# Performance work log

Hardware: AMD Instinct MI355X
Metric: run time of the kernel (lower is better)

## Reference

```python
import jax, jax.numpy as jnp
import numpy as np

NU, NM, FEAT, E, EL, H, ED, C = 50000, 20000, 32, 262144, 100000, 512, 7, 7


def _seg_mean(msg, dst, n):
    # scatter-mean aggregation (PyG SAGEConv default aggr='mean'; empty segments -> 0)
    s = jax.ops.segment_sum(msg, dst, num_segments=n)
    cnt = jax.ops.segment_sum(jnp.ones(dst.shape, msg.dtype), dst, num_segments=n)
    return s / jnp.maximum(cnt, 1.0)[:, None]


def _conv(x_src, x_dst, ei, ea, lw, lb, rw, ew, eb):
    # EdgeSAGEConv: message = x_j + edge_lin(edge_attr); out = lin_l(mean-aggr) + lin_r(x_dst)
    msg = x_src[ei[0]] + ea @ ew + eb            # [E, H]
    agg = _seg_mean(msg, ei[1], x_dst.shape[0])  # [N_dst, H]
    return agg @ lw + lb + x_dst @ rw


def setup_inputs() -> dict:
    key = jax.random.key(0)
    ks = iter(jax.random.split(key, 40))

    def rn(shape, scale=1.0):
        return jax.random.normal(next(ks), shape, jnp.float32) * scale

    inp = {}
    inp["movie_x"] = rn((NM, FEAT))
    inp["user_emb_w"] = rn((NU, H))
    inp["movie_emb_w"] = rn((NM, H))
    inp["movie_lin_w"] = rn((FEAT, H), FEAT ** -0.5)
    inp["movie_lin_b"] = jnp.zeros((H,), jnp.float32)
    inp["edge_attr_um"] = rn((E, ED))
    inp["edge_attr_mu"] = rn((E, ED))
    for p in ("mu1", "um1", "mu2", "um2"):
        inp[p + "_lin_l_w"] = rn((H, H), H ** -0.5)
        inp[p + "_lin_l_b"] = jnp.zeros((H,), jnp.float32)
        inp[p + "_lin_r_w"] = rn((H, H), H ** -0.5)
        inp[p + "_edge_w"] = rn((ED, H), ED ** -0.5)
        inp[p + "_edge_b"] = jnp.zeros((H,), jnp.float32)
    inp["cls_w"] = rn((2 * H, C), (2 * H) ** -0.5)
    inp["cls_b"] = jnp.zeros((C,), jnp.float32)
    inp["edge_index_um"] = jnp.stack([
        jax.random.randint(next(ks), (E,), 0, NU),
        jax.random.randint(next(ks), (E,), 0, NM)])
    inp["edge_index_mu"] = jnp.stack([
        jax.random.randint(next(ks), (E,), 0, NM),
        jax.random.randint(next(ks), (E,), 0, NU)])
    inp["edge_label_index"] = jnp.stack([
        jax.random.randint(next(ks), (EL,), 0, NU),
        jax.random.randint(next(ks), (EL,), 0, NM)])
    return inp


def reference(movie_x, user_emb_w, movie_emb_w, movie_lin_w, movie_lin_b,
              edge_attr_um, edge_attr_mu,
              mu1_lin_l_w, mu1_lin_l_b, mu1_lin_r_w, mu1_edge_w, mu1_edge_b,
              um1_lin_l_w, um1_lin_l_b, um1_lin_r_w, um1_edge_w, um1_edge_b,
              mu2_lin_l_w, mu2_lin_l_b, mu2_lin_r_w, mu2_edge_w, mu2_edge_b,
              um2_lin_l_w, um2_lin_l_b, um2_lin_r_w, um2_edge_w, um2_edge_b,
              cls_w, cls_b,
              edge_index_um, edge_index_mu, edge_label_index):
    # node encoders (node_id == arange -> embedding table used directly)
    x_u = user_emb_w                                             # [NU, H]
    x_m = movie_x @ movie_lin_w + movie_lin_b + movie_emb_w      # [NM, H]
    # hetero layer 1 (one edge type per destination node type)
    u1 = jax.nn.relu(_conv(x_m, x_u, edge_index_mu, edge_attr_mu,
                           mu1_lin_l_w, mu1_lin_l_b, mu1_lin_r_w, mu1_edge_w, mu1_edge_b))
    m1 = jax.nn.relu(_conv(x_u, x_m, edge_index_um, edge_attr_um,
                           um1_lin_l_w, um1_lin_l_b, um1_lin_r_w, um1_edge_w, um1_edge_b))
    # hetero layer 2
    u2 = _conv(m1, u1, edge_index_mu, edge_attr_mu,
               mu2_lin_l_w, mu2_lin_l_b, mu2_lin_r_w, mu2_edge_w, mu2_edge_b)
    m2 = _conv(u1, m1, edge_index_um, edge_attr_um,
               um2_lin_l_w, um2_lin_l_b, um2_lin_r_w, um2_edge_w, um2_edge_b)
    # edge classifier
    feat = jnp.concatenate([u2[edge_label_index[0]], m2[edge_label_index[1]]], axis=-1)
    return feat @ cls_w + cls_b
```

## Files before the change

kernel.cpp:

```cpp
#include <hip/hip_runtime.h>
#include <hip/hip_bf16.h>

#define NUU 50000
#define NMM 20000
#define NT (NUU + NMM)
#define FEAT 32
#define NE 262144
#define NEL 100000
#define HD 512
#define EDIM 7
#define NC 7

typedef __hip_bfloat16 bf16;
typedef __attribute__((ext_vector_type(8))) short short8;
typedef __attribute__((ext_vector_type(4))) float f32x4;

__device__ __forceinline__ float b2f(unsigned short u)
{
  return __uint_as_float((unsigned)u << 16);
}
__device__ __forceinline__ unsigned short f2bbits(float x)
{
  __hip_bfloat16 h = __float2bfloat16(x);
  return *reinterpret_cast<unsigned short*>(&h);
}
__device__ __forceinline__ float2 ld2(const float* p) { return *(const float2*)p; }
__device__ __forceinline__ void st2b(bf16* p, float x, float y)
{
  ushort2 u = make_ushort2(f2bbits(x), f2bbits(y));
  *(ushort2*)p = u;
}
__device__ __forceinline__ void gload16(const void* g, void* l)
{
  __builtin_amdgcn_global_load_lds(
      (const __attribute__((address_space(1))) void*)g,
      (__attribute__((address_space(3))) void*)l, 16, 0, 0);
}

__global__ __launch_bounds__(256) void prep_k(
    const float* __restrict__ mx, const float* __restrict__ W,
    const float* __restrict__ b, const float* __restrict__ emb,
    bf16* __restrict__ xm, const float* __restrict__ uin, bf16* __restrict__ ubf)
{
  const int tid = threadIdx.x;
  if (blockIdx.x < 1024) {
    const int c0 = 2 * tid;
    float2 wreg[FEAT];
#pragma unroll
    for (int k = 0; k < FEAT; ++k) wreg[k] = ld2(&W[(size_t)k * HD + c0]);
    const float2 bv = ld2(&b[c0]);
    __shared__ float xr[FEAT];
    for (int m = blockIdx.x; m < NMM; m += 1024) {
      if (tid < FEAT) xr[tid] = mx[(size_t)m * FEAT + tid];
      __syncthreads();
      float2 e2 = ld2(&emb[(size_t)m * HD + c0]);
      float s0 = bv.x + e2.x, s1 = bv.y + e2.y;
#pragma unroll
      for (int k = 0; k < FEAT; ++k) {
        s0 += xr[k] * wreg[k].x;
        s1 += xr[k] * wreg[k].y;
      }
      st2b(&xm[(size_t)m * HD + c0], s0, s1);
      __syncthreads();
    }
  } else {
    const int n4 = NUU * HD / 4;
    for (int i = (blockIdx.x - 1024) * 256 + tid; i < n4; i += 1024 * 256) {
      float4 v = *(const float4*)&uin[4 * (size_t)i];
      ushort4 u = make_ushort4(f2bbits(v.x), f2bbits(v.y), f2bbits(v.z), f2bbits(v.w));
      *(ushort4*)&ubf[4 * (size_t)i] = u;
    }
  }
}

__global__ __launch_bounds__(256) void wtrans_k(
    const float* __restrict__ lwA, const float* __restrict__ rwA, bf16* __restrict__ WcA,
    const float* __restrict__ lwB, const float* __restrict__ rwB, bf16* __restrict__ WcB)
{
  const float* lw = blockIdx.z ? lwB : lwA;
  const float* rw = blockIdx.z ? rwB : rwA;
  bf16* Wcat = blockIdx.z ? WcB : WcA;
  __shared__ float s[32][33];
  const int tx = threadIdx.x & 31;
  const int ty = threadIdx.x >> 5;
  const int nt = blockIdx.x * 32;
  const int kt = blockIdx.y * 32;
#pragma unroll
  for (int q = 0; q < 4; ++q) {
    int k = kt + q * 8 + ty;
    int n = nt + tx;
    float v = (k < HD) ? lw[(size_t)k * HD + n] : rw[(size_t)(k - HD) * HD + n];
    s[q * 8 + ty][tx] = v;
  }
  __syncthreads();
#pragma unroll
  for (int q = 0; q < 4; ++q) {
    int n = nt + q * 8 + ty;
    int k = kt + tx;
    Wcat[(size_t)n * (2 * HD) + k] = __float2bfloat16(s[tx][q * 8 + ty]);
  }
}

__global__ void count2_k(const int* __restrict__ dmu, const int* __restrict__ dum,
                         int* __restrict__ cnt)
{
  for (int i = blockIdx.x * blockDim.x + threadIdx.x; i < NE; i += gridDim.x * blockDim.x) {
    atomicAdd(&cnt[dmu[i]], 1);
    atomicAdd(&cnt[NUU + dum[i]], 1);
  }
}

__global__ __launch_bounds__(512) void scan_a512(const int* __restrict__ in,
                                                 int* __restrict__ out,
                                                 int* __restrict__ bsum, int n)
{
  __shared__ int s[512];
  const int tid = threadIdx.x;
  const int i = blockIdx.x * 512 + tid;
  int v = (i < n) ? in[i] : 0;
  s[tid] = v;
  __syncthreads();
  for (int d = 1; d < 512; d <<= 1) {
    int t = (tid >= d) ? s[tid - d] : 0;
    __syncthreads();
    s[tid] += t;
    __syncthreads();
  }
  if (i < n) out[i] = s[tid] - v;
  if (tid == 511) bsum[blockIdx.x] = s[511];
}

__global__ void scan_b256(int* __restrict__ bsum, int nb)
{
  __shared__ int s[256];
  const int tid = threadIdx.x;
  int v = (tid < nb) ? bsum[tid] : 0;
  s[tid] = v;
  __syncthreads();
  for (int d = 1; d < 256; d <<= 1) {
    int t = (tid >= d) ? s[tid - d] : 0;
    __syncthreads();
    s[tid] += t;
    __syncthreads();
  }
  if (tid < nb) bsum[tid] = s[tid] - v;
}

__global__ __launch_bounds__(512) void scan_c512(int* __restrict__ out,
                                                 const int* __restrict__ bsum, int n)
{
  const int i = blockIdx.x * 512 + threadIdx.x;
  if (i < n) out[i] += bsum[blockIdx.x];
}

__global__ void fill2_k(const int* __restrict__ smu, const int* __restrict__ dmu,
                        const int* __restrict__ sum_, const int* __restrict__ dum,
                        const int* __restrict__ off, int* __restrict__ fill,
                        int* __restrict__ csrE, int* __restrict__ csrS)
{
  for (int i = blockIdx.x * blockDim.x + threadIdx.x; i < NE; i += gridDim.x * blockDim.x) {
    int d0 = dmu[i];
    int p0 = off[d0] + atomicAdd(&fill[d0], 1);
    csrE[p0] = i;
    csrS[p0] = smu[i];
    int d1 = NUU + dum[i];
    int p1 = off[d1] + atomicAdd(&fill[d1], 1);
    csrE[p1] = i;
    csrS[p1] = sum_[i];
  }
}

__global__ __launch_bounds__(256) void easum2_k(
    const float* __restrict__ eaMU, const float* __restrict__ eaUM,
    const int* __restrict__ csrE, const int* __restrict__ off,
    const int* __restrict__ cnt, float* __restrict__ eaSum)
{
  const int g = threadIdx.x >> 3;
  const int cl = threadIdx.x & 7;
  const int d = blockIdx.x * 32 + g;
  if (d >= NT) return;
  const float* __restrict__ ea = (d < NUU) ? eaMU : eaUM;
  const int deg = cnt[d];
  const int start = off[d];
  float a = 0.f;
  for (int i = 0; i < deg; ++i) {
    int e = csrE[start + i];
    if (cl < 7) a += ea[(size_t)e * EDIM + cl];
  }
  eaSum[(size_t)d * 8 + cl] = (cl < 7) ? a : 0.f;
}

__global__ __launch_bounds__(64) void projw_k(
    const float* __restrict__ lwA, const float* __restrict__ rwA,
    const float* __restrict__ lbA, const float* __restrict__ clsW,
    float* __restrict__ WlA, float* __restrict__ WrA, float* __restrict__ ccA,
    const float* __restrict__ lwB, const float* __restrict__ rwB,
    const float* __restrict__ lbB,
    float* __restrict__ WlB, float* __restrict__ WrB, float* __restrict__ ccB)
{
  const int side = blockIdx.y;
  const float* lw = side ? lwB : lwA;
  const float* rw = side ? rwB : rwA;
  const float* lb = side ? lbB : lbA;
  const float* cw = clsW + (side ? (size_t)HD * NC : 0);
  float* Wl = side ? WlB : WlA;
  float* Wr = side ? WrB : WrA;
  float* cc = side ? ccB : ccA;
  const int k = blockIdx.x;
  const int l = threadIdx.x;
  if (k < HD) {
    float aL[NC] = {0, 0, 0, 0, 0, 0, 0};
    float aR[NC] = {0, 0, 0, 0, 0, 0, 0};
    for (int j = l; j < HD; j += 64) {
      float a = lw[(size_t)k * HD + j];
      float b = rw[(size_t)k * HD + j];
#pragma unroll
      for (int c = 0; c < NC; ++c) {
        float w = cw[(size_t)j * NC + c];
        aL[c] += a * w;
        aR[c] += b * w;
      }
    }
#pragma unroll
    for (int c = 0; c < NC; ++c)
      for (int s = 32; s; s >>= 1) {
        aL[c] += __shfl_xor(aL[c], s);
        aR[c] += __shfl_xor(aR[c], s);
      }
    if (l == 0) {
#pragma unroll
      for (int c = 0; c < NC; ++c) {
        Wl[k * NC + c] = aL[c];
        Wr[k * NC + c] = aR[c];
      }
    }
  } else {
    float a0[NC] = {0, 0, 0, 0, 0, 0, 0};
    for (int j = l; j < HD; j += 64) {
      float a = lb[j];
#pragma unroll
      for (int c = 0; c < NC; ++c) a0[c] += a * cw[(size_t)j * NC + c];
    }
#pragma unroll
    for (int c = 0; c < NC; ++c)
      for (int s = 32; s; s >>= 1) a0[c] += __shfl_xor(a0[c], s);
    if (l == 0) {
#pragma unroll
      for (int c = 0; c < NC; ++c) cc[c] = a0[c];
    }
  }
}

__global__ __launch_bounds__(512) void proj2_k(
    const float* __restrict__ ewA, const float* __restrict__ ebA,
    const float* __restrict__ WlA, float* __restrict__ ewPA, float* __restrict__ ebPA,
    const float* __restrict__ ewB, const float* __restrict__ ebB,
    const float* __restrict__ WlB, float* __restrict__ ewPB, float* __restrict__ ebPB)
{
  const int side = blockIdx.x;
  const float* ew = side ? ewB : ewA;
  const float* ebv = side ? ebB : ebA;
  const float* Wl = side ? WlB : WlA;
  float* ewP = side ? ewPB : ewPA;
  float* ebP = side ? ebPB : ebPA;
  const int j = threadIdx.x >> 6;
  const int l = threadIdx.x & 63;
  const float* __restrict__ src = (j < 7) ? &ew[(size_t)j * HD] : ebv;
  float acc[NC] = {0, 0, 0, 0, 0, 0, 0};
  for (int k = l; k < HD; k += 64) {
    float v = src[k];
#pragma unroll
    for (int c = 0; c < NC; ++c) acc[c] += v * Wl[(size_t)k * NC + c];
  }
#pragma unroll
  for (int c = 0; c < NC; ++c)
    for (int s = 32; s; s >>= 1) acc[c] += __shfl_xor(acc[c], s);
  if (l == 0) {
    if (j < 7) {
#pragma unroll
      for (int c = 0; c < NC; ++c) ewP[j * 8 + c] = acc[c];
      ewP[j * 8 + 7] = 0.f;
    } else {
#pragma unroll
      for (int c = 0; c < NC; ++c) ebP[c] = acc[c];
      ebP[7] = 0.f;
    }
  }
}

__global__ __launch_bounds__(256) void w2t_k(
    const float* __restrict__ WAu, const float* __restrict__ WBu, bf16* __restrict__ W2u,
    const float* __restrict__ WAm, const float* __restrict__ WBm, bf16* __restrict__ W2m)
{
  int idx = blockIdx.x * 256 + threadIdx.x;
  if (idx >= 2 * 16 * HD) return;
  const int side = idx >= 16 * HD;
  if (side) idx -= 16 * HD;
  const float* WA = side ? WAm : WAu;
  const float* WB = side ? WBm : WBu;
  bf16* W2t = side ? W2m : W2u;
  int n = idx >> 9;
  int k = idx & (HD - 1);
  float v = 0.f;
  if (n < 7) v = WA[k * NC + n];
  else if (n >= 8 && n < 15) v = WB[k * NC + (n - 8)];
  W2t[(size_t)n * HD + k] = __float2bfloat16(v);
}

__global__ __launch_bounds__(256) void agg_all_k(
    const float* __restrict__ mPa, const float* __restrict__ uPb,
    const float* __restrict__ uPa, const float* __restrict__ mPb,
    const int* __restrict__ csrS, const int* __restrict__ off,
    const int* __restrict__ cnt, const float* __restrict__ eaSum,
    const float* __restrict__ ewP_u, const float* __restrict__ ebP_u,
    const float* __restrict__ cc_u, const float* __restrict__ ewP_m,
    const float* __restrict__ ebP_m, const float* __restrict__ cc_m,
    float* __restrict__ Pu, float* __restrict__ Pm)
{
  const int g = threadIdx.x >> 3;
  const int cl = threadIdx.x & 7;
  const int d = blockIdx.x * 32 + g;
  if (d >= NT) return;
  const int user = (d < NUU);
  const float* srcP = user ? mPa : uPa;
  const float* ownP = user ? uPb : mPb;
  const float* ewP = user ? ewP_u : ewP_m;
  const float* ebP = user ? ebP_u : ebP_m;
  const float* cc = user ? cc_u : cc_m;
  float* P = user ? Pu : Pm;
  const int dl = user ? d : d - NUU;
  const int deg = cnt[d];
  const int start = off[d];
  float a = 0.f;
  int i = 0;
  for (; i + 1 < deg; i += 2) {
    int s0 = csrS[start + i], s1 = csrS[start + i + 1];
    a += srcP[(size_t)s0 * 8 + cl] + srcP[(size_t)s1 * 8 + cl];
  }
  if (i < deg) a += srcP[(size_t)csrS[start + i] * 8 + cl];
  float r = ownP[(size_t)dl * 8 + cl] + ((cl < 7) ? cc[cl] : 0.f);
  if (deg > 0) {
    float inv = 1.f / (float)deg;
    float es = 0.f;
#pragma unroll
    for (int j = 0; j < NC; ++j) es += eaSum[(size_t)d * 8 + j] * ewP[j * 8 + cl];
    r += (a + es) * inv + ebP[cl];
  }
  if (cl < 7) P[(size_t)dl * NC + cl] = r;
}

__global__ __launch_bounds__(256) void spmm_all_k(
    const bf16* __restrict__ x_m, const bf16* __restrict__ ue_bf,
    const int* __restrict__ csrS, const int* __restrict__ off,
    const int* __restrict__ cnt, const float* __restrict__ eaSum,
    const float* __restrict__ ew_u, const float* __restrict__ eb_u,
    const float* __restrict__ ew_m, const float* __restrict__ eb_m,
    bf16* __restrict__ t)
{
  const int lane = threadIdx.x & 63;
  const int d = blockIdx.x * 4 + (threadIdx.x >> 6);
  if (d >= NT) return;
  const int user = (d < NUU);
  const bf16* __restrict__ xsrc = user ? x_m : ue_bf;
  const float* __restrict__ ew = user ? ew_u : ew_m;
  const float* __restrict__ eb = user ? eb_u : eb_m;
  const int deg = cnt[d];
  const int start = off[d];
  const int c0 = lane * 8;
  float acc[8] = {0.f, 0.f, 0.f, 0.f, 0.f, 0.f, 0.f, 0.f};
  int i = 0;
  for (; i + 3 < deg; i += 4) {
    int s0 = csrS[start + i], s1 = csrS[start + i + 1];
    int s2 = csrS[start + i + 2], s3 = csrS[start + i + 3];
    short8 v0 = *(const short8*)&xsrc[(size_t)s0 * HD + c0];
    short8 v1 = *(const short8*)&xsrc[(size_t)s1 * HD + c0];
    short8 v2 = *(const short8*)&xsrc[(size_t)s2 * HD + c0];
    short8 v3 = *(const short8*)&xsrc[(size_t)s3 * HD + c0];
#pragma unroll
    for (int j = 0; j < 8; ++j)
      acc[j] += (b2f((unsigned short)v0[j]) + b2f((unsigned short)v1[j])) +
                (b2f((unsigned short)v2[j]) + b2f((unsigned short)v3[j]));
  }
  for (; i < deg; ++i) {
    int s = csrS[start + i];
    short8 v = *(const short8*)&xsrc[(size_t)s * HD + c0];
#pragma unroll
    for (int j = 0; j < 8; ++j) acc[j] += b2f((unsigned short)v[j]);
  }
  short8 sv;
  if (deg > 0) {
    const float inv = 1.f / (float)deg;
    float es[8] = {0.f, 0.f, 0.f, 0.f, 0.f, 0.f, 0.f, 0.f};
#pragma unroll
    for (int j = 0; j < NC; ++j) {
      const float av = eaSum[(size_t)d * 8 + j];
      const float* __restrict__ wr = &ew[(size_t)j * HD + c0];
#pragma unroll
      for (int jj = 0; jj < 8; ++jj) es[jj] += av * wr[jj];
    }
#pragma unroll
    for (int jj = 0; jj < 8; ++jj)
      sv[jj] = (short)f2bbits((acc[jj] + es[jj]) * inv + eb[c0 + jj]);
  } else {
#pragma unroll
    for (int jj = 0; jj < 8; ++jj) sv[jj] = (short)f2bbits(0.f);
  }
  *(short8*)&t[(size_t)d * HD + c0] = sv;
}

__global__ __launch_bounds__(256) void gemm_all_k(
    const bf16* __restrict__ tbuf, const bf16* __restrict__ ue_bf,
    const bf16* __restrict__ x_m, const bf16* __restrict__ Wcat_u,
    const bf16* __restrict__ Wcat_m, const float* __restrict__ bias_u,
    const float* __restrict__ bias_m, const bf16* __restrict__ W2t_u,
    const bf16* __restrict__ W2t_m, float* __restrict__ PpU,
    float* __restrict__ PpM, int nwgU)
{
  __shared__ __align__(16) char lds[34816];
  const int tid = threadIdx.x;
  const int lane = tid & 63;
  const int wid = tid >> 6;
  const int wr = wid >> 1, wc = wid & 1;
  const int lr = lane & 15, lk = lane >> 4;

  const int nwg = gridDim.x;
  const int orig = blockIdx.x;
  const int q = nwg >> 3, r8 = nwg & 7;
  const int xcd = orig & 7, pos = orig >> 3;
  const int wg = (xcd < r8) ? xcd * (q + 1) + pos : r8 * (q + 1) + (xcd - r8) * q + pos;

  const int user = (wg < nwgU);
  const int wl = user ? wg : wg - nwgU;
  const bf16* __restrict__ A1 = user ? tbuf : tbuf + (size_t)NUU * HD;
  const bf16* __restrict__ A2 = user ? ue_bf : x_m;
  const bf16* __restrict__ Wcat = user ? Wcat_u : Wcat_m;
  const float* __restrict__ bias = user ? bias_u : bias_m;
  const bf16* __restrict__ W2t = user ? W2t_u : W2t_m;
  float* __restrict__ Ppart = user ? PpU : PpM;
  const int M = user ? NUU : NMM;

  const int mt = wl >> 2, nt = wl & 3;
  const int m0 = mt * 128;
  const int n0 = nt * 128;

  const int srow = tid >> 2;
  const int sslot = tid & 3;

  f32x4 acc[4][4];
#pragma unroll
  for (int i = 0; i < 4; ++i)
#pragma unroll
    for (int j = 0; j < 4; ++j) acc[i][j] = (f32x4){0.f, 0.f, 0.f, 0.f};

  int gr0 = m0 + srow;       if (gr0 >= M) gr0 = M - 1;
  int gr1 = m0 + srow + 64;  if (gr1 >= M) gr1 = M - 1;
  const size_t aoff0 = (size_t)gr0 * HD + 8 * sslot;
  const size_t aoff1 = (size_t)gr1 * HD + 8 * sslot;
  const size_t boff0 = (size_t)(n0 + srow) * (2 * HD) + 8 * sslot;
  const size_t boff1 = (size_t)(n0 + srow + 64) * (2 * HD) + 8 * sslot;

  for (int ks = 0; ks < 32; ++ks) {
    const int k0 = ks * 32;
    const bf16* __restrict__ Ap = (k0 < HD) ? A1 : A2;
    const int ac = k0 & (HD - 1);
    gload16(Ap + aoff0 + ac, &lds[tid * 16]);
    gload16(Ap + aoff1 + ac, &lds[4096 + tid * 16]);
    gload16(Wcat + boff0 + k0, &lds[8192 + tid * 16]);
    gload16(Wcat + boff1 + k0, &lds[12288 + tid * 16]);
    __syncthreads();

    short8 af[4], bfr[4];
#pragma unroll
    for (int mf = 0; mf < 4; ++mf)
      af[mf] = *(const short8*)&lds[(wr * 64 + mf * 16 + lr) * 64 + lk * 16];
#pragma unroll
    for (int nf = 0; nf < 4; ++nf)
      bfr[nf] = *(const short8*)&lds[8192 + (wc * 64 + nf * 16 + lr) * 64 + lk * 16];
#pragma unroll
    for (int mf = 0; mf < 4; ++mf)
#pragma unroll
      for (int nf = 0; nf < 4; ++nf)
        acc[mf][nf] = __builtin_amdgcn_mfma_f32_16x16x32_bf16(
            af[mf], bfr[nf], acc[mf][nf], 0, 0, 0);
    __syncthreads();
  }

  bf16* zs = (bf16*)lds;
  const int ZLD = 136;
#pragma unroll
  for (int nf = 0; nf < 4; ++nf) {
    const int col_l = wc * 64 + nf * 16 + lr;
    const float bv = bias[n0 + col_l];
#pragma unroll
    for (int mf = 0; mf < 4; ++mf) {
      const int row_l = wr * 64 + mf * 16 + lk * 4;
#pragma unroll
      for (int r = 0; r < 4; ++r) {
        float v = fmaxf(acc[mf][nf][r] + bv, 0.f);
        zs[(size_t)(row_l + r) * ZLD + col_l] = __float2bfloat16(v);
      }
    }
  }
  __syncthreads();

  const int strip = wid * 32;
  f32x4 p0 = {0.f, 0.f, 0.f, 0.f}, p1 = {0.f, 0.f, 0.f, 0.f};
#pragma unroll
  for (int kk = 0; kk < 4; ++kk) {
    short8 bfg = *(const short8*)&W2t[(size_t)lr * HD + n0 + kk * 32 + 8 * lk];
    short8 a0 = *(const short8*)&zs[(size_t)(strip + lr) * ZLD + kk * 32 + 8 * lk];
    short8 a1 = *(const short8*)&zs[(size_t)(strip + 16 + lr) * ZLD + kk * 32 + 8 * lk];
    p0 = __builtin_amdgcn_mfma_f32_16x16x32_bf16(a0, bfg, p0, 0, 0, 0);
    p1 = __builtin_amdgcn_mfma_f32_16x16x32_bf16(a1, bfg, p1, 0, 0, 0);
  }
#pragma unroll
  for (int r = 0; r < 4; ++r) {
    int row0 = m0 + strip + lk * 4 + r;
    if (row0 < M) Ppart[((size_t)nt * M + row0) * 16 + lr] = p0[r];
    int row1 = m0 + strip + 16 + lk * 4 + r;
    if (row1 < M) Ppart[((size_t)nt * M + row1) * 16 + lr] = p1[r];
  }
}

__global__ __launch_bounds__(256) void reduce4_k(
    const float* __restrict__ PpU, const float* __restrict__ PpM,
    float* __restrict__ uPa, float* __restrict__ uPb,
    float* __restrict__ mPa, float* __restrict__ mPb)
{
  int idx = blockIdx.x * 256 + threadIdx.x;
  if (idx >= NT * 16) return;
  int row = idx >> 4, j = idx & 15;
  const float* Pp;
  float *Pa, *Pb;
  int rows, r;
  if (row < NUU) { Pp = PpU; Pa = uPa; Pb = uPb; rows = NUU; r = row; }
  else { Pp = PpM; Pa = mPa; Pb = mPb; rows = NMM; r = row - NUU; }
  float s = Pp[((size_t)0 * rows + r) * 16 + j] + Pp[((size_t)1 * rows + r) * 16 + j] +
            Pp[((size_t)2 * rows + r) * 16 + j] + Pp[((size_t)3 * rows + r) * 16 + j];
  if (j < 8) Pa[(size_t)r * 8 + j] = s;
  else Pb[(size_t)r * 8 + (j - 8)] = s;
}

__global__ void gather_out_k(const float* __restrict__ Pu, const float* __restrict__ Pm,
                             const int* __restrict__ eli, const float* __restrict__ cb,
                             float* __restrict__ out)
{
  const int i = blockIdx.x * 256 + threadIdx.x;
  if (i >= NEL * NC) return;
  int e = i / NC;
  int c = i - e * NC;
  out[i] = Pu[(size_t)eli[e] * NC + c] + Pm[(size_t)eli[NEL + e] * NC + c] + cb[c];
}

static inline char* bump(char*& p, size_t bytes)
{
  char* r = p;
  p += (bytes + 255) & ~(size_t)255;
  return r;
}

extern "C" void kernel_launch(void* const* d_in, const int* in_sizes, int n_in,
                              void* d_out, int out_size, void* d_ws, size_t ws_size,
                              hipStream_t stream)
{
  const float* movie_x   = (const float*)d_in[0];
  const float* user_emb  = (const float*)d_in[1];
  const float* movie_emb = (const float*)d_in[2];
  const float* mlw       = (const float*)d_in[3];
  const float* mlb       = (const float*)d_in[4];
  const float* ea_um     = (const float*)d_in[5];
  const float* ea_mu     = (const float*)d_in[6];
  const float* mu1_lw = (const float*)d_in[7];
  const float* mu1_lb = (const float*)d_in[8];
  const float* mu1_rw = (const float*)d_in[9];
  const float* mu1_ew = (const float*)d_in[10];
  const float* mu1_eb = (const float*)d_in[11];
  const float* um1_lw = (const float*)d_in[12];
  const float* um1_lb = (const float*)d_in[13];
  const float* um1_rw = (const float*)d_in[14];
  const float* um1_ew = (const float*)d_in[15];
  const float* um1_eb = (const float*)d_in[16];
  const float* mu2_lw = (const float*)d_in[17];
  const float* mu2_lb = (const float*)d_in[18];
  const float* mu2_rw = (const float*)d_in[19];
  const float* mu2_ew = (const float*)d_in[20];
  const float* mu2_eb = (const float*)d_in[21];
  const float* um2_lw = (const float*)d_in[22];
  const float* um2_lb = (const float*)d_in[23];
  const float* um2_rw = (const float*)d_in[24];
  const float* um2_ew = (const float*)d_in[25];
  const float* um2_eb = (const float*)d_in[26];
  const float* cls_w  = (const float*)d_in[27];
  const float* cls_b  = (const float*)d_in[28];
  const int*   ei_um  = (const int*)d_in[29];
  const int*   ei_mu  = (const int*)d_in[30];
  const int*   eli    = (const int*)d_in[31];
  float* out = (float*)d_out;

  char* w = (char*)d_ws;
  bf16* x_m   = (bf16*)bump(w, (size_t)NMM * HD * 2);
  bf16* tbuf  = (bf16*)bump(w, (size_t)NT * HD * 2);
  bf16* ue_bf = (bf16*)bump(w, (size_t)NUU * HD * 2);
  bf16* Wcat_u1 = (bf16*)bump(w, (size_t)HD * 2 * HD * 2);
  bf16* Wcat_m1 = (bf16*)bump(w, (size_t)HD * 2 * HD * 2);
  float* PpU  = (float*)bump(w, (size_t)4 * NUU * 16 * 4);
  float* PpM  = (float*)bump(w, (size_t)4 * NMM * 16 * 4);
  float* uPa  = (float*)bump(w, (size_t)NUU * 8 * 4);
  float* uPb  = (float*)bump(w, (size_t)NUU * 8 * 4);
  float* mPa  = (float*)bump(w, (size_t)NMM * 8 * 4);
  float* mPb  = (float*)bump(w, (size_t)NMM * 8 * 4);
  float* Pu   = (float*)bump(w, (size_t)NUU * NC * 4);
  float* Pm   = (float*)bump(w, (size_t)NMM * NC * 4);
  float* Wl_u = (float*)bump(w, (size_t)HD * NC * 4);
  float* Wr_u = (float*)bump(w, (size_t)HD * NC * 4);
  float* cc_u = (float*)bump(w, 64 * 4);
  float* Wl_m = (float*)bump(w, (size_t)HD * NC * 4);
  float* Wr_m = (float*)bump(w, (size_t)HD * NC * 4);
  float* cc_m = (float*)bump(w, 64 * 4);
  bf16* W2t_u = (bf16*)bump(w, (size_t)16 * HD * 2);
  bf16* W2t_m = (bf16*)bump(w, (size_t)16 * HD * 2);
  float* eaSum = (float*)bump(w, (size_t)NT * 8 * 4);
  float* ewP_u = (float*)bump(w, 64 * 4);
  float* ebP_u = (float*)bump(w, 64 * 4);
  float* ewP_m = (float*)bump(w, 64 * 4);
  float* ebP_m = (float*)bump(w, 64 * 4);
  int* cf     = (int*)bump(w, (size_t)2 * NT * 4);
  int* cnt    = cf;
  int* fill   = cf + NT;
  int* off    = (int*)bump(w, (size_t)NT * 4);
  int* bsum   = (int*)bump(w, 256 * 4);
  int* csrE   = (int*)bump(w, (size_t)2 * NE * 4);
  int* csrS   = (int*)bump(w, (size_t)2 * NE * 4);

  const int GN = (NT + 511) / 512;

  hipMemsetAsync(cf, 0, (size_t)2 * NT * 4, stream);

  prep_k<<<2048, 256, 0, stream>>>(movie_x, mlw, mlb, movie_emb, x_m, user_emb, ue_bf);
  {
    dim3 g(HD / 32, 2 * HD / 32, 2);
    wtrans_k<<<g, 256, 0, stream>>>(mu1_lw, mu1_rw, Wcat_u1, um1_lw, um1_rw, Wcat_m1);
  }

  count2_k<<<1024, 256, 0, stream>>>(ei_mu + NE, ei_um + NE, cnt);
  scan_a512<<<GN, 512, 0, stream>>>(cnt, off, bsum, NT);
  scan_b256<<<1, 256, 0, stream>>>(bsum, GN);
  scan_c512<<<GN, 512, 0, stream>>>(off, bsum, NT);
  fill2_k<<<1024, 256, 0, stream>>>(ei_mu, ei_mu + NE, ei_um, ei_um + NE,
                                    off, fill, csrE, csrS);
  easum2_k<<<(NT + 31) / 32, 256, 0, stream>>>(ea_mu, ea_um, csrE, off, cnt, eaSum);

  {
    dim3 g(HD + 1, 2);
    projw_k<<<g, 64, 0, stream>>>(mu2_lw, mu2_rw, mu2_lb, cls_w, Wl_u, Wr_u, cc_u,
                                  um2_lw, um2_rw, um2_lb, Wl_m, Wr_m, cc_m);
  }
  proj2_k<<<2, 512, 0, stream>>>(mu2_ew, mu2_eb, Wl_u, ewP_u, ebP_u,
                                 um2_ew, um2_eb, Wl_m, ewP_m, ebP_m);
  w2t_k<<<64, 256, 0, stream>>>(Wl_m, Wr_u, W2t_u, Wl_u, Wr_m, W2t_m);

  spmm_all_k<<<(NT + 3) / 4, 256, 0, stream>>>(x_m, ue_bf, csrS, off, cnt, eaSum,
                                               mu1_ew, mu1_eb, um1_ew, um1_eb, tbuf);
  const int nwgU = ((NUU + 127) / 128) * 4;
  const int nwgM = ((NMM + 127) / 128) * 4;
  gemm_all_k<<<nwgU + nwgM, 256, 0, stream>>>(tbuf, ue_bf, x_m, Wcat_u1, Wcat_m1,
                                              mu1_lb, um1_lb, W2t_u, W2t_m,
                                              PpU, PpM, nwgU);

  reduce4_k<<<(NT * 16 + 255) / 256, 256, 0, stream>>>(PpU, PpM, uPa, uPb, mPa, mPb);

  agg_all_k<<<(NT + 31) / 32, 256, 0, stream>>>(mPa, uPb, uPa, mPb, csrS, off, cnt,
                                                eaSum, ewP_u, ebP_u, cc_u,
                                                ewP_m, ebP_m, cc_m, Pu, Pm);

  gather_out_k<<<(NEL * NC + 255) / 256, 256, 0, stream>>>(Pu, Pm, eli, cls_b, out);
}
```

Baseline: 361.3 us.

## Fuse edge-attr sums into count pass and atomically reduce GEMM partials

Edge-attribute per-destination sums are now accumulated with float atomics inside the degree-count pass, which removes the csrE array and the separate easum kernel. The GEMM epilogue atomically adds its four N-tile partials into a single zeroed Pab buffer, so the reduce4 kernel and the partial buffers are gone, and agg reads Pab directly. The proj2 and w2t kernels are merged into one launch. In exchange, many float atomics are added, including contended ones on popular destinations, and summation order becomes nondeterministic.

```diff
diff --git a/kernel.cpp b/kernel.cpp
--- a/kernel.cpp
+++ b/kernel.cpp
@@ -101,12 +101,20 @@
   }
 }
 
-__global__ void count2_k(const int* __restrict__ dmu, const int* __restrict__ dum,
-                         int* __restrict__ cnt)
+__global__ void edge_pass_k(const int* __restrict__ dmu, const int* __restrict__ dum,
+                            const float* __restrict__ eaMU, const float* __restrict__ eaUM,
+                            int* __restrict__ cnt, float* __restrict__ eaSum)
 {
   for (int i = blockIdx.x * blockDim.x + threadIdx.x; i < NE; i += gridDim.x * blockDim.x) {
-    atomicAdd(&cnt[dmu[i]], 1);
-    atomicAdd(&cnt[NUU + dum[i]], 1);
+    int d0 = dmu[i];
+    int d1 = NUU + dum[i];
+    atomicAdd(&cnt[d0], 1);
+    atomicAdd(&cnt[d1], 1);
+#pragma unroll
+    for (int c = 0; c < NC; ++c) {
+      atomicAdd(&eaSum[(size_t)d0 * 8 + c], eaMU[(size_t)i * EDIM + c]);
+      atomicAdd(&eaSum[(size_t)d1 * 8 + c], eaUM[(size_t)i * EDIM + c]);
+    }
   }
 }
 
@@ -156,38 +164,16 @@
 __global__ void fill2_k(const int* __restrict__ smu, const int* __restrict__ dmu,
                         const int* __restrict__ sum_, const int* __restrict__ dum,
                         const int* __restrict__ off, int* __restrict__ fill,
-                        int* __restrict__ csrE, int* __restrict__ csrS)
+                        int* __restrict__ csrS)
 {
   for (int i = blockIdx.x * blockDim.x + threadIdx.x; i < NE; i += gridDim.x * blockDim.x) {
     int d0 = dmu[i];
     int p0 = off[d0] + atomicAdd(&fill[d0], 1);
-    csrE[p0] = i;
     csrS[p0] = smu[i];
     int d1 = NUU + dum[i];
     int p1 = off[d1] + atomicAdd(&fill[d1], 1);
-    csrE[p1] = i;
     csrS[p1] = sum_[i];
   }
-}
-
-__global__ __launch_bounds__(256) void easum2_k(
-    const float* __restrict__ eaMU, const float* __restrict__ eaUM,
-    const int* __restrict__ csrE, const int* __restrict__ off,
-    const int* __restrict__ cnt, float* __restrict__ eaSum)
-{
-  const int g = threadIdx.x >> 3;
-  const int cl = threadIdx.x & 7;
-  const int d = blockIdx.x * 32 + g;
-  if (d >= NT) return;
-  const float* __restrict__ ea = (d < NUU) ? eaMU : eaUM;
-  const int deg = cnt[d];
-  const int start = off[d];
-  float a = 0.f;
-  for (int i = 0; i < deg; ++i) {
-    int e = csrE[start + i];
-    if (cl < 7) a += ea[(size_t)e * EDIM + cl];
-  }
-  eaSum[(size_t)d * 8 + cl] = (cl < 7) ? a : 0.f;
 }
 
 __global__ __launch_bounds__(64) void projw_k(
@@ -251,67 +237,65 @@
   }
 }
 
-__global__ __launch_bounds__(512) void proj2_k(
+__global__ __launch_bounds__(256) void p2w2t_k(
     const float* __restrict__ ewA, const float* __restrict__ ebA,
     const float* __restrict__ WlA, float* __restrict__ ewPA, float* __restrict__ ebPA,
     const float* __restrict__ ewB, const float* __restrict__ ebB,
-    const float* __restrict__ WlB, float* __restrict__ ewPB, float* __restrict__ ebPB)
-{
-  const int side = blockIdx.x;
-  const float* ew = side ? ewB : ewA;
-  const float* ebv = side ? ebB : ebA;
-  const float* Wl = side ? WlB : WlA;
-  float* ewP = side ? ewPB : ewPA;
-  float* ebP = side ? ebPB : ebPA;
-  const int j = threadIdx.x >> 6;
-  const int l = threadIdx.x & 63;
-  const float* __restrict__ src = (j < 7) ? &ew[(size_t)j * HD] : ebv;
-  float acc[NC] = {0, 0, 0, 0, 0, 0, 0};
-  for (int k = l; k < HD; k += 64) {
-    float v = src[k];
-#pragma unroll
-    for (int c = 0; c < NC; ++c) acc[c] += v * Wl[(size_t)k * NC + c];
-  }
-#pragma unroll
-  for (int c = 0; c < NC; ++c)
-    for (int s = 32; s; s >>= 1) acc[c] += __shfl_xor(acc[c], s);
-  if (l == 0) {
-    if (j < 7) {
-#pragma unroll
-      for (int c = 0; c < NC; ++c) ewP[j * 8 + c] = acc[c];
-      ewP[j * 8 + 7] = 0.f;
-    } else {
-#pragma unroll
-      for (int c = 0; c < NC; ++c) ebP[c] = acc[c];
-      ebP[7] = 0.f;
-    }
-  }
-}
-
-__global__ __launch_bounds__(256) void w2t_k(
+    const float* __restrict__ WlB, float* __restrict__ ewPB, float* __restrict__ ebPB,
     const float* __restrict__ WAu, const float* __restrict__ WBu, bf16* __restrict__ W2u,
     const float* __restrict__ WAm, const float* __restrict__ WBm, bf16* __restrict__ W2m)
 {
-  int idx = blockIdx.x * 256 + threadIdx.x;
-  if (idx >= 2 * 16 * HD) return;
-  const int side = idx >= 16 * HD;
-  if (side) idx -= 16 * HD;
-  const float* WA = side ? WAm : WAu;
-  const float* WB = side ? WBm : WBu;
-  bf16* W2t = side ? W2m : W2u;
-  int n = idx >> 9;
-  int k = idx & (HD - 1);
-  float v = 0.f;
-  if (n < 7) v = WA[k * NC + n];
-  else if (n >= 8 && n < 15) v = WB[k * NC + (n - 8)];
-  W2t[(size_t)n * HD + k] = __float2bfloat16(v);
+  const int b = blockIdx.x;
+  if (b < 4) {
+    const int side = b >> 1;
+    const float* ew = side ? ewB : ewA;
+    const float* ebv = side ? ebB : ebA;
+    const float* Wl = side ? WlB : WlA;
+    float* ewP = side ? ewPB : ewPA;
+    float* ebP = side ? ebPB : ebPA;
+    const int j = (b & 1) * 4 + (threadIdx.x >> 6);
+    const int l = threadIdx.x & 63;
+    const float* __restrict__ src = (j < 7) ? &ew[(size_t)j * HD] : ebv;
+    float acc[NC] = {0, 0, 0, 0, 0, 0, 0};
+    for (int k = l; k < HD; k += 64) {
+      float v = src[k];
+#pragma unroll
+      for (int c = 0; c < NC; ++c) acc[c] += v * Wl[(size_t)k * NC + c];
+    }
+#pragma unroll
+    for (int c = 0; c < NC; ++c)
+      for (int s = 32; s; s >>= 1) acc[c] += __shfl_xor(acc[c], s);
+    if (l == 0) {
+      if (j < 7) {
+#pragma unroll
+        for (int c = 0; c < NC; ++c) ewP[j * 8 + c] = acc[c];
+        ewP[j * 8 + 7] = 0.f;
+      } else {
+#pragma unroll
+        for (int c = 0; c < NC; ++c) ebP[c] = acc[c];
+        ebP[7] = 0.f;
+      }
+    }
+  } else {
+    int idx = (b - 4) * 256 + threadIdx.x;
+    const int side = idx >= 16 * HD;
+    if (side) idx -= 16 * HD;
+    const float* WA = side ? WAm : WAu;
+    const float* WB = side ? WBm : WBu;
+    bf16* W2t = side ? W2m : W2u;
+    int n = idx >> 9;
+    int k = idx & (HD - 1);
+    float v = 0.f;
+    if (n < 7) v = WA[k * NC + n];
+    else if (n >= 8 && n < 15) v = WB[k * NC + (n - 8)];
+    W2t[(size_t)n * HD + k] = __float2bfloat16(v);
+  }
 }
 
 __global__ __launch_bounds__(256) void agg_all_k(
-    const float* __restrict__ mPa, const float* __restrict__ uPb,
-    const float* __restrict__ uPa, const float* __restrict__ mPb,
-    const int* __restrict__ csrS, const int* __restrict__ off,
-    const int* __restrict__ cnt, const float* __restrict__ eaSum,
+    const float* __restrict__ Pab, const int* __restrict__ csrS,
+    const int* __restrict__ off, const int* __restrict__ cnt,
+    const float* __restrict__ eaSum,
     const float* __restrict__ ewP_u, const float* __restrict__ ebP_u,
     const float* __restrict__ cc_u, const float* __restrict__ ewP_m,
     const float* __restrict__ ebP_m, const float* __restrict__ cc_m,
@@ -322,8 +306,7 @@
   const int d = blockIdx.x * 32 + g;
   if (d >= NT) return;
   const int user = (d < NUU);
-  const float* srcP = user ? mPa : uPa;
-  const float* ownP = user ? uPb : mPb;
+  const size_t srcbase = user ? (size_t)NUU : 0;
   const float* ewP = user ? ewP_u : ewP_m;
   const float* ebP = user ? ebP_u : ebP_m;
   const float* cc = user ? cc_u : cc_m;
@@ -335,10 +318,10 @@
   int i = 0;
   for (; i + 1 < deg; i += 2) {
     int s0 = csrS[start + i], s1 = csrS[start + i + 1];
-    a += srcP[(size_t)s0 * 8 + cl] + srcP[(size_t)s1 * 8 + cl];
-  }
-  if (i < deg) a += srcP[(size_t)csrS[start + i] * 8 + cl];
-  float r = ownP[(size_t)dl * 8 + cl] + ((cl < 7) ? cc[cl] : 0.f);
+    a += Pab[(srcbase + s0) * 16 + cl] + Pab[(srcbase + s1) * 16 + cl];
+  }
+  if (i < deg) a += Pab[(srcbase + csrS[start + i]) * 16 + cl];
+  float r = Pab[(size_t)d * 16 + 8 + cl] + ((cl < 7) ? cc[cl] : 0.f);
   if (deg > 0) {
     float inv = 1.f / (float)deg;
     float es = 0.f;
@@ -413,8 +396,7 @@
     const bf16* __restrict__ x_m, const bf16* __restrict__ Wcat_u,
     const bf16* __restrict__ Wcat_m, const float* __restrict__ bias_u,
     const float* __restrict__ bias_m, const bf16* __restrict__ W2t_u,
-    const bf16* __restrict__ W2t_m, float* __restrict__ PpU,
-    float* __restrict__ PpM, int nwgU)
+    const bf16* __restrict__ W2t_m, float* __restrict__ Pab, int nwgU)
 {
   __shared__ __align__(16) char lds[34816];
   const int tid = threadIdx.x;
@@ -436,8 +418,8 @@
   const bf16* __restrict__ Wcat = user ? Wcat_u : Wcat_m;
   const float* __restrict__ bias = user ? bias_u : bias_m;
   const bf16* __restrict__ W2t = user ? W2t_u : W2t_m;
-  float* __restrict__ Ppart = user ? PpU : PpM;
   const int M = user ? NUU : NMM;
+  const size_t rowbase = user ? 0 : (size_t)NUU;
 
   const int mt = wl >> 2, nt = wl & 3;
   const int m0 = mt * 128;
@@ -516,29 +498,10 @@
 #pragma unroll
   for (int r = 0; r < 4; ++r) {
     int row0 = m0 + strip + lk * 4 + r;
-    if (row0 < M) Ppart[((size_t)nt * M + row0) * 16 + lr] = p0[r];
+    if (row0 < M) atomicAdd(&Pab[(rowbase + row0) * 16 + lr], p0[r]);
     int row1 = m0 + strip + 16 + lk * 4 + r;
-    if (row1 < M) Ppart[((size_t)nt * M + row1) * 16 + lr] = p1[r];
-  }
-}
-
-__global__ __launch_bounds__(256) void reduce4_k(
-    const float* __restrict__ PpU, const float* __restrict__ PpM,
-    float* __restrict__ uPa, float* __restrict__ uPb,
-    float* __restrict__ mPa, float* __restrict__ mPb)
-{
-  int idx = blockIdx.x * 256 + threadIdx.x;
-  if (idx >= NT * 16) return;
-  int row = idx >> 4, j = idx & 15;
-  const float* Pp;
-  float *Pa, *Pb;
-  int rows, r;
-  if (row < NUU) { Pp = PpU; Pa = uPa; Pb = uPb; rows = NUU; r = row; }
-  else { Pp = PpM; Pa = mPa; Pb = mPb; rows = NMM; r = row - NUU; }
-  float s = Pp[((size_t)0 * rows + r) * 16 + j] + Pp[((size_t)1 * rows + r) * 16 + j] +
-            Pp[((size_t)2 * rows + r) * 16 + j] + Pp[((size_t)3 * rows + r) * 16 + j];
-  if (j < 8) Pa[(size_t)r * 8 + j] = s;
-  else Pb[(size_t)r * 8 + (j - 8)] = s;
+    if (row1 < M) atomicAdd(&Pab[(rowbase + row1) * 16 + lr], p1[r]);
+  }
 }
 
 __global__ void gather_out_k(const float* __restrict__ Pu, const float* __restrict__ Pm,
@@ -598,17 +561,18 @@
   float* out = (float*)d_out;
 
   char* w = (char*)d_ws;
+  char* zbase = w;
+  int* cf     = (int*)bump(w, (size_t)2 * NT * 4);
+  int* cnt    = cf;
+  int* fill   = cf + NT;
+  float* Pab  = (float*)bump(w, (size_t)NT * 16 * 4);
+  float* eaSum = (float*)bump(w, (size_t)NT * 8 * 4);
+  size_t zbytes = (size_t)(w - zbase);
   bf16* x_m   = (bf16*)bump(w, (size_t)NMM * HD * 2);
   bf16* tbuf  = (bf16*)bump(w, (size_t)NT * HD * 2);
   bf16* ue_bf = (bf16*)bump(w, (size_t)NUU * HD * 2);
   bf16* Wcat_u1 = (bf16*)bump(w, (size_t)HD * 2 * HD * 2);
   bf16* Wcat_m1 = (bf16*)bump(w, (size_t)HD * 2 * HD * 2);
-  float* PpU  = (float*)bump(w, (size_t)4 * NUU * 16 * 4);
-  float* PpM  = (float*)bump(w, (size_t)4 * NMM * 16 * 4);
-  float* uPa  = (float*)bump(w, (size_t)NUU * 8 * 4);
-  float* uPb  = (float*)bump(w, (size_t)NUU * 8 * 4);
-  float* mPa  = (float*)bump(w, (size_t)NMM * 8 * 4);
-  float* mPb  = (float*)bump(w, (size_t)NMM * 8 * 4);
   float* Pu   = (float*)bump(w, (size_t)NUU * NC * 4);
   float* Pm   = (float*)bump(w, (size_t)NMM * NC * 4);
   float* Wl_u = (float*)bump(w, (size_t)HD * NC * 4);
@@ -619,22 +583,17 @@
   float* cc_m = (float*)bump(w, 64 * 4);
   bf16* W2t_u = (bf16*)bump(w, (size_t)16 * HD * 2);
   bf16* W2t_m = (bf16*)bump(w, (size_t)16 * HD * 2);
-  float* eaSum = (float*)bump(w, (size_t)NT * 8 * 4);
   float* ewP_u = (float*)bump(w, 64 * 4);
   float* ebP_u = (float*)bump(w, 64 * 4);
   float* ewP_m = (float*)bump(w, 64 * 4);
   float* ebP_m = (float*)bump(w, 64 * 4);
-  int* cf     = (int*)bump(w, (size_t)2 * NT * 4);
-  int* cnt    = cf;
-  int* fill   = cf + NT;
   int* off    = (int*)bump(w, (size_t)NT * 4);
   int* bsum   = (int*)bump(w, 256 * 4);
-  int* csrE   = (int*)bump(w, (size_t)2 * NE * 4);
   int* csrS   = (int*)bump(w, (size_t)2 * NE * 4);
 
   const int GN = (NT + 511) / 512;
 
-  hipMemsetAsync(cf, 0, (size_t)2 * NT * 4, stream);
+  hipMemsetAsync(zbase, 0, zbytes, stream);
 
   prep_k<<<2048, 256, 0, stream>>>(movie_x, mlw, mlb, movie_emb, x_m, user_emb, ue_bf);
   {
@@ -642,22 +601,21 @@
     wtrans_k<<<g, 256, 0, stream>>>(mu1_lw, mu1_rw, Wcat_u1, um1_lw, um1_rw, Wcat_m1);
   }
 
-  count2_k<<<1024, 256, 0, stream>>>(ei_mu + NE, ei_um + NE, cnt);
+  edge_pass_k<<<1024, 256, 0, stream>>>(ei_mu + NE, ei_um + NE, ea_mu, ea_um, cnt, eaSum);
   scan_a512<<<GN, 512, 0, stream>>>(cnt, off, bsum, NT);
   scan_b256<<<1, 256, 0, stream>>>(bsum, GN);
   scan_c512<<<GN, 512, 0, stream>>>(off, bsum, NT);
   fill2_k<<<1024, 256, 0, stream>>>(ei_mu, ei_mu + NE, ei_um, ei_um + NE,
-                                    off, fill, csrE, csrS);
-  easum2_k<<<(NT + 31) / 32, 256, 0, stream>>>(ea_mu, ea_um, csrE, off, cnt, eaSum);
+                                    off, fill, csrS);
 
   {
     dim3 g(HD + 1, 2);
     projw_k<<<g, 64, 0, stream>>>(mu2_lw, mu2_rw, mu2_lb, cls_w, Wl_u, Wr_u, cc_u,
                                   um2_lw, um2_rw, um2_lb, Wl_m, Wr_m, cc_m);
   }
-  proj2_k<<<2, 512, 0, stream>>>(mu2_ew, mu2_eb, Wl_u, ewP_u, ebP_u,
-                                 um2_ew, um2_eb, Wl_m, ewP_m, ebP_m);
-  w2t_k<<<64, 256, 0, stream>>>(Wl_m, Wr_u, W2t_u, Wl_u, Wr_m, W2t_m);
+  p2w2t_k<<<68, 256, 0, stream>>>(mu2_ew, mu2_eb, Wl_u, ewP_u, ebP_u,
+                                  um2_ew, um2_eb, Wl_m, ewP_m, ebP_m,
+                                  Wl_m, Wr_u, W2t_u, Wl_u, Wr_m, W2t_m);
 
   spmm_all_k<<<(NT + 3) / 4, 256, 0, stream>>>(x_m, ue_bf, csrS, off, cnt, eaSum,
                                                mu1_ew, mu1_eb, um1_ew, um1_eb, tbuf);
@@ -665,12 +623,10 @@
   const int nwgM = ((NMM + 127) / 128) * 4;
   gemm_all_k<<<nwgU + nwgM, 256, 0, stream>>>(tbuf, ue_bf, x_m, Wcat_u1, Wcat_m1,
                                               mu1_lb, um1_lb, W2t_u, W2t_m,
-                                              PpU, PpM, nwgU);
-
-  reduce4_k<<<(NT * 16 + 255) / 256, 256, 0, stream>>>(PpU, PpM, uPa, uPb, mPa, mPb);
-
-  agg_all_k<<<(NT + 31) / 32, 256, 0, stream>>>(mPa, uPb, uPa, mPb, csrS, off, cnt,
-                                                eaSum, ewP_u, ebP_u, cc_u,
+                                              Pab, nwgU);
+
+  agg_all_k<<<(NT + 31) / 32, 256, 0, stream>>>(Pab, csrS, off, cnt, eaSum,
+                                                ewP_u, ebP_u, cc_u,
                                                 ewP_m, ebP_m, cc_m, Pu, Pm);
 
   gather_out_k<<<(NEL * NC + 255) / 256, 256, 0, stream>>>(Pu, Pm, eli, cls_b, out);
```

After: 515.0 us. 42.5% more time.
